# Kernel optimization log

Hardware: AMD Instinct MI355X
Metric: run time of the kernel (lower is better)

Reference implementation:

```python
import jax, jax.numpy as jnp
import numpy as np


def setup_inputs() -> dict:
    key = jax.random.key(0)
    k1, k2 = jax.random.split(key)
    T, R, C = 4096, 4096, 1
    output = jax.random.normal(k1, (T, R, C), dtype=jnp.float32)
    results = jax.random.randint(k2, (T, R, C), 0, 2, dtype=jnp.int32)
    return {"output": output, "results": results}


def _mean_squared_increment(p, s):
    # p: [T, R] float predictions (channel 0); s: [T, R] int rain sign.
    # Runs: consecutive day-pairs where sign is unchanged; a sign change
    # flushes the current run's mean and resets. Final loss = mean of run means.
    same = s[1:] == s[:-1]                      # [T-1, R] pair kept?
    sq = jnp.square(p[1:] - p[:-1])             # [T-1, R] squared increment
    T1, R = same.shape
    # New run starts at every 'different' pair; inclusive cumsum gives each
    # boundary element a fresh id shared with the following 'same' pairs.
    boundary = (~same).astype(jnp.int32)
    seg_local = jnp.cumsum(boundary, axis=0)    # values in [0, T1]
    offsets = jnp.arange(R, dtype=jnp.int32)[None, :] * (T1 + 1)
    seg = (seg_local + offsets).ravel()
    num_segments = (T1 + 1) * R
    w = same.astype(sq.dtype)
    sums = jax.ops.segment_sum((sq * w).ravel(), seg, num_segments=num_segments)
    cnts = jax.ops.segment_sum(w.ravel(), seg, num_segments=num_segments)
    valid = cnts > 0
    means = jnp.where(valid, sums / jnp.where(valid, cnts, 1.0), 0.0)
    n_valid = valid.sum().astype(sq.dtype)
    return jnp.where(n_valid > 0, means.sum() / jnp.maximum(n_valid, 1.0), 0.0)


def reference(output, results):
    p0 = output[:, :, 0]
    t0 = results[:, :, 0]
    return _mean_squared_increment(p0, t0)
```

## Files before the change

kernel.cpp:

```cpp
#include <hip/hip_runtime.h>

#define COLS 4096
#define C4   (COLS / 4)
#define TROWS 4096
#define PAIRS (TROWS - 1)

struct Rec { float hs, hc, ts, tc, ms, mc, ao; };

__device__ inline Rec rec_merge(const Rec& L, const Rec& R) {
    Rec o;
    if (L.ao != 0.f && R.ao != 0.f) {
        o.hs = L.hs + R.hs; o.hc = L.hc + R.hc;
        o.ts = o.hs;        o.tc = o.hc;
        o.ms = 0.f; o.mc = 0.f; o.ao = 1.f;
    } else if (L.ao != 0.f) {
        o.hs = L.hs + R.hs; o.hc = L.hc + R.hc;
        o.ts = R.ts; o.tc = R.tc;
        o.ms = R.ms; o.mc = R.mc; o.ao = 0.f;
    } else if (R.ao != 0.f) {
        o.hs = L.hs; o.hc = L.hc;
        o.ts = L.ts + R.hs; o.tc = L.tc + R.hc;
        o.ms = L.ms; o.mc = L.mc; o.ao = 0.f;
    } else {
        o.hs = L.hs; o.hc = L.hc;
        o.ts = R.ts; o.tc = R.tc;
        float js = L.ts + R.hs, jc = L.tc + R.hc;
        bool v = jc > 0.f;
        o.ms = L.ms + R.ms + (v ? js / jc : 0.f);
        o.mc = L.mc + R.mc + (v ? 1.f : 0.f);
        o.ao = 0.f;
    }
    return o;
}

__device__ inline Rec rec_load(const float4* base, size_t idx) {
    float4 a = base[idx * 2], b = base[idx * 2 + 1];
    Rec r; r.hs = a.x; r.hc = a.y; r.ts = a.z; r.tc = a.w;
    r.ms = b.x; r.mc = b.y; r.ao = b.z; return r;
}
__device__ inline void rec_store(float4* base, size_t idx, const Rec& r) {
    base[idx * 2]     = make_float4(r.hs, r.hc, r.ts, r.tc);
    base[idx * 2 + 1] = make_float4(r.ms, r.mc, r.ao, 0.f);
}

__global__ void msi_phase1(const float4* __restrict__ p4, const int4* __restrict__ s4,
                           float4* __restrict__ recs, int NC, int PCH) {
    int g = blockIdx.x * blockDim.x + threadIdx.x;
    int c = blockIdx.y;
    int t0 = c * PCH;
    int t1 = t0 + PCH; if (t1 > PAIRS) t1 = PAIRS;

    float4 pp = p4[(size_t)t0 * C4 + g];
    int4   sp = s4[(size_t)t0 * C4 + g];
    float pprev[4] = {pp.x, pp.y, pp.z, pp.w};
    int   sprev[4] = {sp.x, sp.y, sp.z, sp.w};

    float cs[4] = {0.f, 0.f, 0.f, 0.f};
    int   cc[4] = {0, 0, 0, 0};
    float hs[4] = {0.f, 0.f, 0.f, 0.f};
    int   hc[4] = {0, 0, 0, 0};
    int   hd[4] = {0, 0, 0, 0};
    float ms[4] = {0.f, 0.f, 0.f, 0.f};
    int   mc[4] = {0, 0, 0, 0};

#define PROC(PV, SV)                                                          \
    {                                                                         \
        float pcur[4] = {(PV).x, (PV).y, (PV).z, (PV).w};                     \
        int   scur[4] = {(SV).x, (SV).y, (SV).z, (SV).w};                     \
        _Pragma("unroll")                                                     \
        for (int k = 0; k < 4; ++k) {                                         \
            float d = pcur[k] - pprev[k];                                     \
            bool same = (scur[k] == sprev[k]);                                \
            bool first = !same && !hd[k];                                     \
            bool interior = !same && hd[k] && (cc[k] > 0);                    \
            hs[k] = first ? cs[k] : hs[k];                                    \
            hc[k] = first ? cc[k] : hc[k];                                    \
            float mean = cs[k] * __builtin_amdgcn_rcpf((float)cc[k]);         \
            ms[k] += interior ? mean : 0.f;                                   \
            mc[k] += interior ? 1 : 0;                                        \
            hd[k] = hd[k] | (same ? 0 : 1);                                   \
            cs[k] = same ? cs[k] + d * d : 0.f;                               \
            cc[k] = same ? cc[k] + 1 : 0;                                     \
            pprev[k] = pcur[k];                                               \
            sprev[k] = scur[k];                                               \
        }                                                                     \
    }

    int n = t1 - t0;
    int nb = n >> 2;
    size_t base = (size_t)(t0 + 1) * C4 + g;
    const size_t stride = 4 * (size_t)C4;

    if (nb > 0) {
        float4 P0 = p4[base], P1 = p4[base + C4], P2 = p4[base + 2 * C4], P3 = p4[base + 3 * C4];
        int4   S0 = s4[base], S1 = s4[base + C4], S2 = s4[base + 2 * C4], S3 = s4[base + 3 * C4];
        base += stride;
        #pragma unroll 2
        for (int b = 0; b < nb - 1; ++b) {
            float4 Q0 = p4[base], Q1 = p4[base + C4], Q2 = p4[base + 2 * C4], Q3 = p4[base + 3 * C4];
            int4   T0 = s4[base], T1 = s4[base + C4], T2 = s4[base + 2 * C4], T3 = s4[base + 3 * C4];
            base += stride;
            PROC(P0, S0); PROC(P1, S1); PROC(P2, S2); PROC(P3, S3);
            P0 = Q0; P1 = Q1; P2 = Q2; P3 = Q3;
            S0 = T0; S1 = T1; S2 = T2; S3 = T3;
        }
        PROC(P0, S0); PROC(P1, S1); PROC(P2, S2); PROC(P3, S3);
    }
    for (int t = t0 + (nb << 2); t < t1; ++t) {
        size_t bb = (size_t)(t + 1) * C4 + g;
        float4 P0 = p4[bb];
        int4   S0 = s4[bb];
        PROC(P0, S0);
    }
#undef PROC

    #pragma unroll
    for (int k = 0; k < 4; ++k) {
        int r = 4 * g + k;
        Rec rec;
        if (!hd[k]) {
            rec.hs = cs[k]; rec.hc = (float)cc[k];
            rec.ts = cs[k]; rec.tc = (float)cc[k];
            rec.ms = 0.f; rec.mc = 0.f; rec.ao = 1.f;
        } else {
            rec.hs = hs[k]; rec.hc = (float)hc[k];
            rec.ts = cs[k]; rec.tc = (float)cc[k];
            rec.ms = ms[k]; rec.mc = (float)mc[k]; rec.ao = 0.f;
        }
        rec_store(recs, (size_t)c * COLS + r, rec);
    }
}

__global__ void msi_phase2a(const float4* __restrict__ recs, float4* __restrict__ supers,
                            int G) {
    int r = blockIdx.x * blockDim.x + threadIdx.x;
    int sup = blockIdx.y;
    size_t base = (size_t)sup * G * COLS + r;
    Rec acc = rec_load(recs, base);
    #pragma unroll 4
    for (int j = 1; j < G; ++j) {
        Rec nxt = rec_load(recs, base + (size_t)j * COLS);
        acc = rec_merge(acc, nxt);
    }
    rec_store(supers, (size_t)sup * COLS + r, acc);
}

__global__ void msi_phase2b(const float4* __restrict__ supers, double* __restrict__ partials,
                            int NSUP) {
    int r = blockIdx.x * blockDim.x + threadIdx.x;
    Rec acc = rec_load(supers, r);
    for (int j = 1; j < NSUP; ++j)
        acc = rec_merge(acc, rec_load(supers, (size_t)j * COLS + r));

    double msum, mcnt;
    if (acc.ao != 0.f) {
        bool v = acc.hc > 0.f;
        msum = v ? (double)(acc.hs / acc.hc) : 0.0;
        mcnt = v ? 1.0 : 0.0;
    } else {
        msum = (double)acc.ms; mcnt = (double)acc.mc;
        if (acc.hc > 0.f) { msum += (double)(acc.hs / acc.hc); mcnt += 1.0; }
        if (acc.tc > 0.f) { msum += (double)(acc.ts / acc.tc); mcnt += 1.0; }
    }

    __shared__ double ls[256];
    __shared__ double lc[256];
    int tid = threadIdx.x;
    ls[tid] = msum; lc[tid] = mcnt;
    __syncthreads();
    for (int off = 128; off > 0; off >>= 1) {
        if (tid < off) { ls[tid] += ls[tid + off]; lc[tid] += lc[tid + off]; }
        __syncthreads();
    }
    if (tid == 0) {
        partials[blockIdx.x * 2 + 0] = ls[0];
        partials[blockIdx.x * 2 + 1] = lc[0];
    }
}

__global__ void msi_phase3(const double* __restrict__ partials, int nparts,
                           float* __restrict__ out) {
    int tid = threadIdx.x;
    double msum = 0.0, mcnt = 0.0;
    if (tid < nparts) {
        msum = partials[tid * 2 + 0];
        mcnt = partials[tid * 2 + 1];
    }
    for (int off = 32; off > 0; off >>= 1) {
        msum += __shfl_down(msum, off);
        mcnt += __shfl_down(mcnt, off);
    }
    if (tid == 0) out[0] = (mcnt > 0.0) ? (float)(msum / mcnt) : 0.f;
}

extern "C" void kernel_launch(void* const* d_in, const int* in_sizes, int n_in,
                              void* d_out, int out_size, void* d_ws, size_t ws_size,
                              hipStream_t stream) {
    const float4* p = (const float4*)d_in[0];
    const int4*   s = (const int4*)d_in[1];
    float* out = (float*)d_out;

    const int nblocks2 = COLS / 256;
    int NC = 128;
    auto need = [&](int nc) -> size_t {
        int gg = nc < 16 ? nc : 16;
        int nsup = nc / gg;
        return (size_t)(nc + nsup) * COLS * 32 + (size_t)nblocks2 * 2 * sizeof(double);
    };
    while (NC > 1 && need(NC) > ws_size) NC >>= 1;
    int G = NC < 16 ? NC : 16;
    int NSUP = NC / G;
    int PCH = (PAIRS + NC - 1) / NC;

    float4* recs     = (float4*)d_ws;
    float4* supers   = recs + (size_t)NC * COLS * 2;
    double* partials = (double*)(supers + (size_t)NSUP * COLS * 2);

    dim3 g1(C4 / 256, NC);
    msi_phase1<<<g1, 256, 0, stream>>>(p, s, recs, NC, PCH);
    dim3 g2a(COLS / 256, NSUP);
    msi_phase2a<<<g2a, 256, 0, stream>>>(recs, supers, G);
    msi_phase2b<<<nblocks2, 256, 0, stream>>>(supers, partials, NSUP);
    msi_phase3<<<1, 64, 0, stream>>>(partials, nblocks2, out);
}
```

Before: 52.77 us.

## Pack chunk records into 16 bytes and double the number of time chunks

Each per-chunk scan record is now one float4: three float sums plus three 10-bit counts and the all-same flag bit-packed into the fourth word, instead of two float4s. With records half the size, the chunk count rises from 128 to 256 at about the same workspace traffic, so phase 1 launches twice as many blocks over shorter time ranges. A launch-bounds hint is added to phase 1. The risk is that the 10-bit count fields overflow if the chunk length ever exceeds 1023, and that a longer phase-2a reduction offsets the gain.

```diff
diff --git a/kernel.cpp b/kernel.cpp
--- a/kernel.cpp
+++ b/kernel.cpp
@@ -33,18 +33,31 @@
     return o;
 }
 
-__device__ inline Rec rec_load(const float4* base, size_t idx) {
+__device__ inline Rec rec16_load(const float4* base, size_t idx) {
+    float4 a = base[idx];
+    unsigned u = __float_as_uint(a.w);
+    Rec r;
+    r.hs = a.x; r.ts = a.y; r.ms = a.z;
+    r.hc = (float)(u & 1023u);
+    r.tc = (float)((u >> 10) & 1023u);
+    r.mc = (float)((u >> 20) & 1023u);
+    r.ao = (float)(u >> 30);
+    return r;
+}
+
+__device__ inline Rec rec32_load(const float4* base, size_t idx) {
     float4 a = base[idx * 2], b = base[idx * 2 + 1];
     Rec r; r.hs = a.x; r.hc = a.y; r.ts = a.z; r.tc = a.w;
     r.ms = b.x; r.mc = b.y; r.ao = b.z; return r;
 }
-__device__ inline void rec_store(float4* base, size_t idx, const Rec& r) {
+__device__ inline void rec32_store(float4* base, size_t idx, const Rec& r) {
     base[idx * 2]     = make_float4(r.hs, r.hc, r.ts, r.tc);
     base[idx * 2 + 1] = make_float4(r.ms, r.mc, r.ao, 0.f);
 }
 
-__global__ void msi_phase1(const float4* __restrict__ p4, const int4* __restrict__ s4,
-                           float4* __restrict__ recs, int NC, int PCH) {
+__global__ __launch_bounds__(256, 4)
+void msi_phase1(const float4* __restrict__ p4, const int4* __restrict__ s4,
+                float4* __restrict__ recs, int NC, int PCH) {
     int g = blockIdx.x * blockDim.x + threadIdx.x;
     int c = blockIdx.y;
     int t0 = c * PCH;
@@ -117,17 +130,16 @@
     #pragma unroll
     for (int k = 0; k < 4; ++k) {
         int r = 4 * g + k;
-        Rec rec;
+        float4 a;
         if (!hd[k]) {
-            rec.hs = cs[k]; rec.hc = (float)cc[k];
-            rec.ts = cs[k]; rec.tc = (float)cc[k];
-            rec.ms = 0.f; rec.mc = 0.f; rec.ao = 1.f;
+            unsigned u = (unsigned)cc[k] | ((unsigned)cc[k] << 10) | (3u << 30);
+            a = make_float4(cs[k], cs[k], 0.f, __uint_as_float(u));
         } else {
-            rec.hs = hs[k]; rec.hc = (float)hc[k];
-            rec.ts = cs[k]; rec.tc = (float)cc[k];
-            rec.ms = ms[k]; rec.mc = (float)mc[k]; rec.ao = 0.f;
+            unsigned u = (unsigned)hc[k] | ((unsigned)cc[k] << 10) |
+                         ((unsigned)mc[k] << 20);
+            a = make_float4(hs[k], cs[k], ms[k], __uint_as_float(u));
         }
-        rec_store(recs, (size_t)c * COLS + r, rec);
+        recs[(size_t)c * COLS + r] = a;
     }
 }
 
@@ -136,21 +148,21 @@
     int r = blockIdx.x * blockDim.x + threadIdx.x;
     int sup = blockIdx.y;
     size_t base = (size_t)sup * G * COLS + r;
-    Rec acc = rec_load(recs, base);
+    Rec acc = rec16_load(recs, base);
     #pragma unroll 4
     for (int j = 1; j < G; ++j) {
-        Rec nxt = rec_load(recs, base + (size_t)j * COLS);
+        Rec nxt = rec16_load(recs, base + (size_t)j * COLS);
         acc = rec_merge(acc, nxt);
     }
-    rec_store(supers, (size_t)sup * COLS + r, acc);
+    rec32_store(supers, (size_t)sup * COLS + r, acc);
 }
 
 __global__ void msi_phase2b(const float4* __restrict__ supers, double* __restrict__ partials,
                             int NSUP) {
     int r = blockIdx.x * blockDim.x + threadIdx.x;
-    Rec acc = rec_load(supers, r);
+    Rec acc = rec32_load(supers, r);
     for (int j = 1; j < NSUP; ++j)
-        acc = rec_merge(acc, rec_load(supers, (size_t)j * COLS + r));
+        acc = rec_merge(acc, rec32_load(supers, (size_t)j * COLS + r));
 
     double msum, mcnt;
     if (acc.ao != 0.f) {
@@ -201,19 +213,20 @@
     float* out = (float*)d_out;
 
     const int nblocks2 = COLS / 256;
-    int NC = 128;
+    int NC = 256;
     auto need = [&](int nc) -> size_t {
         int gg = nc < 16 ? nc : 16;
         int nsup = nc / gg;
-        return (size_t)(nc + nsup) * COLS * 32 + (size_t)nblocks2 * 2 * sizeof(double);
+        return (size_t)nc * COLS * 16 + (size_t)nsup * COLS * 32 +
+               (size_t)nblocks2 * 2 * sizeof(double);
     };
-    while (NC > 1 && need(NC) > ws_size) NC >>= 1;
+    while (NC > 8 && need(NC) > ws_size) NC >>= 1;
     int G = NC < 16 ? NC : 16;
     int NSUP = NC / G;
     int PCH = (PAIRS + NC - 1) / NC;
 
     float4* recs     = (float4*)d_ws;
-    float4* supers   = recs + (size_t)NC * COLS * 2;
+    float4* supers   = recs + (size_t)NC * COLS;
     double* partials = (double*)(supers + (size_t)NSUP * COLS * 2);
 
     dim3 g1(C4 / 256, NC);
```

Result: slower. 59.93 us (+13.6%).
